# Kernel tuning notes

Measured on AMD Instinct MI355X. Metric: run time of the kernel, lower is better.

Reference implementation:

```python
import jax, jax.numpy as jnp
from jax import lax
import numpy as np

N_BLOCKS = 5; C = 256; K = 1024; NQ = 8; NRES = 4; B = 2; T = 65536


def conv1d(x, w, b, stride=1, padding=0, dilation=1):
    # x: [N,C,T], w: [O,I,k]
    y = lax.conv_general_dilated(x, w, (stride,), [(padding, padding)],
                                 rhs_dilation=(dilation,),
                                 dimension_numbers=('NCH', 'OIH', 'NCH'))
    return y + b[None, :, None]


def conv_transpose1d(x, w, b):
    # PyTorch ConvTranspose1d(k=4, s=2, p=1); w: [in, out, 4]
    wk = jnp.swapaxes(jnp.flip(w, -1), 0, 1)  # [out, in, 4]
    y = lax.conv_general_dilated(x, wk, (1,), [(2, 2)], lhs_dilation=(2,),
                                 dimension_numbers=('NCH', 'OIH', 'NCH'))
    return y + b[None, :, None]


def residual_model(x, w0, b0, w1, b1, dil):
    # ReLU -> dilated conv3 -> ReLU -> conv3
    h = conv1d(jax.nn.relu(x), w0, b0, padding=dil, dilation=dil)
    h = conv1d(jax.nn.relu(h), w1, b1, padding=1)
    return h


def encoder(x, d0w, d0b, dw, db, rw, rb):
    for i in range(N_BLOCKS):
        if i == 0:
            x = conv1d(x, d0w, d0b, stride=2, padding=1)
        else:
            x = conv1d(x, dw[i - 1], db[i - 1], stride=2, padding=1)
        for j in range(NRES):
            dil = 3 ** (j + 1)
            # ResidualBlock.forward: x + model(x)
            x = x + residual_model(x, rw[i, j, 0], rb[i, j, 0], rw[i, j, 1], rb[i, j, 1], dil)
    return x


def decoder(x, rw, rb, uw, ub, ulw, ulb):
    for i in range(N_BLOCKS):
        for j in range(NRES):
            dil = 3 ** (j + 1)
            # DecoderBlock: x = x + ResidualBlock(x) = x + (x + model(x))
            x = x + (x + residual_model(x, rw[i, j, 0], rb[i, j, 0], rw[i, j, 1], rb[i, j, 1], dil))
        if i == N_BLOCKS - 1:
            x = conv_transpose1d(x, ulw, ulb)
        else:
            x = conv_transpose1d(x, uw[i], ub[i])
    return x


def rvq(emb, rvq_sum, rvq_usage):
    # emb: [N, C]; eval-mode residual VQ (no EMA update)
    q = jnp.zeros_like(emb)
    commit = jnp.asarray(0.0, emb.dtype)
    codes = []
    for i in range(NQ):
        cb = rvq_sum[i] / jnp.clip(rvq_usage[i], 1e-5, None)[:, None]  # [K, C]
        res = emb - q
        # argmin of squared distance over codebook rows (||res||^2 constant per column)
        scores = jnp.sum(cb * cb, axis=1)[:, None] - 2.0 * (cb @ res.T)  # [K, N]
        c = jnp.argmin(scores, axis=0)
        eq = cb[c]  # [N, C]
        eq_st = res + lax.stop_gradient(eq - res)  # straight-through
        commit = commit + jnp.mean((lax.stop_gradient(eq_st) - res) ** 2)
        q = q + eq_st
        codes.append(c.astype(jnp.int32))
    return jnp.stack(codes, axis=1), q, commit


def setup_inputs() -> dict:
    key = jax.random.key(0)
    ks = iter(jax.random.split(key, 16))

    def W(shape, fan_in):
        return (jax.random.normal(next(ks), shape, jnp.float32) / np.float32(np.sqrt(fan_in)))

    return {
        'x': jax.random.normal(next(ks), (B, 1, T), jnp.float32),
        'enc_down0_w': W((C, 1, 4), 4),
        'enc_down0_b': jnp.zeros((C,), jnp.float32),
        'enc_down_w': W((N_BLOCKS - 1, C, C, 4), C * 4),
        'enc_down_b': jnp.zeros((N_BLOCKS - 1, C), jnp.float32),
        'enc_res_w': W((N_BLOCKS, NRES, 2, C, C, 3), C * 3),
        'enc_res_b': jnp.zeros((N_BLOCKS, NRES, 2, C), jnp.float32),
        'dec_res_w': W((N_BLOCKS, NRES, 2, C, C, 3), C * 3),
        'dec_res_b': jnp.zeros((N_BLOCKS, NRES, 2, C), jnp.float32),
        'dec_up_w': W((N_BLOCKS - 1, C, C, 4), C * 4),
        'dec_up_b': jnp.zeros((N_BLOCKS - 1, C), jnp.float32),
        'dec_up_last_w': W((C, 1, 4), C * 4),
        'dec_up_last_b': jnp.zeros((1,), jnp.float32),
        'rvq_sum': jax.random.normal(next(ks), (NQ, K, C), jnp.float32) * 0.1,
        'rvq_usage': jnp.ones((NQ, K), jnp.float32),
    }


def reference(x, enc_down0_w, enc_down0_b, enc_down_w, enc_down_b, enc_res_w, enc_res_b,
              dec_res_w, dec_res_b, dec_up_w, dec_up_b, dec_up_last_w, dec_up_last_b,
              rvq_sum, rvq_usage):
    z = encoder(x, enc_down0_w, enc_down0_b, enc_down_w, enc_down_b, enc_res_w, enc_res_b)
    Bz, Cz, Tz = z.shape
    emb = jnp.transpose(z, (0, 2, 1)).reshape(Bz * Tz, Cz)  # (b t) c
    codes, q, commit = rvq(emb, rvq_sum, rvq_usage)
    zq = jnp.transpose(q.reshape(Bz, Tz, Cz), (0, 2, 1))  # b c t
    recon = decoder(zq, dec_res_w, dec_res_b, dec_up_w, dec_up_b, dec_up_last_w, dec_up_last_b)
    return recon, codes, commit
```

## Files before the change

kernel.cpp:

```cpp
#include <hip/hip_runtime.h>
#include <cstdint>

#define DEVFN static __device__ __forceinline__
typedef unsigned short ushort_t;
typedef unsigned int uint_t;
typedef short short8 __attribute__((ext_vector_type(8)));
typedef float f32x4 __attribute__((ext_vector_type(4)));

DEVFN float bf2f(ushort_t h) { return __uint_as_float(((uint_t)h) << 16); }
DEVFN ushort_t bfhi(float f) {
    uint_t u = __float_as_uint(f);
    u += 0x7fffu + ((u >> 16) & 1u);
    return (ushort_t)(u >> 16);
}
DEVFN void fsplit(float f, ushort_t& h, ushort_t& l) {
    h = bfhi(f);
    l = bfhi(f - bf2f(h));
}
DEVFN void relu_pair(uint_t& h, uint_t& l) {
    float f0 = bf2f((ushort_t)(h & 0xffffu)) + bf2f((ushort_t)(l & 0xffffu));
    float f1 = bf2f((ushort_t)(h >> 16)) + bf2f((ushort_t)(l >> 16));
    if (f0 <= 0.f) { h &= 0xffff0000u; l &= 0xffff0000u; }
    if (f1 <= 0.f) { h &= 0x0000ffffu; l &= 0x0000ffffu; }
}

__global__ __launch_bounds__(256)
void wprep3_k(const float* __restrict__ erw, const float* __restrict__ drw,
              ushort_t* __restrict__ wH, ushort_t* __restrict__ wL)
{
    const int gid = blockIdx.x * 256 + threadIdx.x;
    const int conv = gid >> 16;
    const int rem  = gid & 65535;
    const int co = rem >> 8, ci = rem & 255;
    const float* src = (conv < 40) ? (erw + (size_t)conv * 196608)
                                   : (drw + (size_t)(conv - 40) * 196608);
    const float* p = src + ((size_t)co * 256 + ci) * 3;
    ushort_t* oh = wH + (size_t)conv * 196608 + rem;
    ushort_t* ol = wL + (size_t)conv * 196608 + rem;
#pragma unroll
    for (int k = 0; k < 3; ++k) {
        ushort_t h, l; fsplit(p[k], h, l);
        oh[k * 65536] = h; ol[k * 65536] = l;
    }
}

__global__ __launch_bounds__(256)
void wprep4_k(const float* __restrict__ edw, const float* __restrict__ duw,
              ushort_t* __restrict__ wH, ushort_t* __restrict__ wL)
{
    const int gid = blockIdx.x * 256 + threadIdx.x;
    const int conv = gid >> 16;
    const int rem  = gid & 65535;
    const int co = rem >> 8, ci = rem & 255;
    ushort_t* oh = wH + (size_t)conv * 262144 + rem;
    ushort_t* ol = wL + (size_t)conv * 262144 + rem;
#pragma unroll
    for (int k = 0; k < 4; ++k) {
        float f;
        if (conv < 4)  f = edw[(size_t)conv * 262144 + ((size_t)co * 256 + ci) * 4 + k];
        else           f = duw[(size_t)(conv - 4) * 262144 + ((size_t)ci * 256 + co) * 4 + k];
        ushort_t h, l; fsplit(f, h, l);
        oh[k * 65536] = h; ol[k * 65536] = l;
    }
}

template<int TAPS, int STRIDE, bool RELU, int NT, int DMAX>
__global__ __launch_bounds__(256, (NT >= 8) ? 2 : 3)
void convs_k(const ushort_t* __restrict__ inH, const ushort_t* __restrict__ inL,
             const ushort_t* __restrict__ wH, const ushort_t* __restrict__ wL,
             const float* __restrict__ bias,
             const ushort_t* __restrict__ srcH, const ushort_t* __restrict__ srcL,
             float alpha,
             ushort_t* __restrict__ outH, ushort_t* __restrict__ outL,
             int Lin, int Lout, int dil, int pad)
{
    constexpr int ROWS = NT * 16;
    constexpr int SMAX = STRIDE * (ROWS - 1) + (TAPS - 1) * DMAX + 1;
    constexpr int XSB  = SMAX * 40 * 2;
    constexpr int ARENA = (2 * XSB > 16640) ? 2 * XSB : 16640;
    __shared__ __align__(16) char sarena[ARENA];
    ushort_t (*xsH)[40] = (ushort_t(*)[40])(sarena);
    ushort_t (*xsL)[40] = (ushort_t(*)[40])(sarena + XSB);

    const int tid = threadIdx.x;
    const int b = blockIdx.z;
    const int t0 = blockIdx.x * ROWS;
    const int wave = tid >> 6, lane = tid & 63;
    const int quad = lane >> 4, lr = lane & 15;
    const int cow = wave * 64;
    const size_t inbase = (size_t)b * Lin * 256;
    const int S = STRIDE * (ROWS - 1) + (TAPS - 1) * dil + 1;
    const int g0 = STRIDE * t0 - pad;

    f32x4 acc[4][NT];
#pragma unroll
    for (int m = 0; m < 4; ++m)
#pragma unroll
        for (int n = 0; n < NT; ++n) acc[m][n] = (f32x4)0.f;

    for (int chunk = 0; chunk < 8; ++chunk) {
        const int ci0 = chunk * 32;
        __syncthreads();
        for (int idx = tid; idx < S * 4; idx += 256) {
            const int s = idx >> 2, p = idx & 3;
            const int t = g0 + s;
            uint4 hv = make_uint4(0, 0, 0, 0), lv = hv;
            if (t >= 0 && t < Lin) {
                const size_t g = inbase + (size_t)t * 256 + ci0 + p * 8;
                hv = *(const uint4*)(inH + g);
                lv = *(const uint4*)(inL + g);
                if (RELU) {
                    relu_pair(hv.x, lv.x); relu_pair(hv.y, lv.y);
                    relu_pair(hv.z, lv.z); relu_pair(hv.w, lv.w);
                }
            }
            *(uint4*)&xsH[s][p * 8] = hv;
            *(uint4*)&xsL[s][p * 8] = lv;
        }
        __syncthreads();
#pragma unroll
        for (int tap = 0; tap < TAPS; ++tap) {
            const ushort_t* wHt = wH + (size_t)tap * 65536 + ci0 + quad * 8;
            const ushort_t* wLt = wL + (size_t)tap * 65536 + ci0 + quad * 8;
            short8 aH[4], aL[4];
#pragma unroll
            for (int m = 0; m < 4; ++m) {
                const int co = cow + m * 16 + lr;
                aH[m] = *(const short8*)(wHt + co * 256);
                aL[m] = *(const short8*)(wLt + co * 256);
            }
            const int rb = tap * dil;
#pragma unroll
            for (int n = 0; n < NT; ++n) {
                const int srow = STRIDE * (n * 16 + lr) + rb;
                const short8 bH = *(const short8*)&xsH[srow][quad * 8];
                const short8 bL = *(const short8*)&xsL[srow][quad * 8];
#pragma unroll
                for (int m = 0; m < 4; ++m)
                    acc[m][n] = __builtin_amdgcn_mfma_f32_16x16x32_bf16(aH[m], bH, acc[m][n], 0, 0, 0);
#pragma unroll
                for (int m = 0; m < 4; ++m)
                    acc[m][n] = __builtin_amdgcn_mfma_f32_16x16x32_bf16(aH[m], bL, acc[m][n], 0, 0, 0);
#pragma unroll
                for (int m = 0; m < 4; ++m)
                    acc[m][n] = __builtin_amdgcn_mfma_f32_16x16x32_bf16(aL[m], bH, acc[m][n], 0, 0, 0);
            }
        }
    }
    float4 bvv[4];
#pragma unroll
    for (int m = 0; m < 4; ++m)
        bvv[m] = *(const float4*)&bias[cow + m * 16 + quad * 4];
    __syncthreads();
    float (*ebuf)[260] = (float(*)[260])sarena;
#pragma unroll
    for (int n = 0; n < NT; ++n) {
#pragma unroll
        for (int m = 0; m < 4; ++m) {
            float4 v;
            v.x = acc[m][n][0] + bvv[m].x;
            v.y = acc[m][n][1] + bvv[m].y;
            v.z = acc[m][n][2] + bvv[m].z;
            v.w = acc[m][n][3] + bvv[m].w;
            *(float4*)&ebuf[lr][cow + m * 16 + quad * 4] = v;
        }
        __syncthreads();
        {
            const int row = tid >> 4;
            const int c00 = (tid & 15) * 4;
            const int t = t0 + n * 16 + row;
            const size_t gr = ((size_t)b * Lout + t) * 256;
#pragma unroll
            for (int rep = 0; rep < 4; ++rep) {
                const int col = c00 + rep * 64;
                float4 v = *(const float4*)&ebuf[row][col];
                if (alpha != 0.f) {
                    const ushort4 sh = *(const ushort4*)(srcH + gr + col);
                    const ushort4 sl = *(const ushort4*)(srcL + gr + col);
                    v.x += alpha * (bf2f(sh.x) + bf2f(sl.x));
                    v.y += alpha * (bf2f(sh.y) + bf2f(sl.y));
                    v.z += alpha * (bf2f(sh.z) + bf2f(sl.z));
                    v.w += alpha * (bf2f(sh.w) + bf2f(sl.w));
                }
                ushort4 oh, ol;
                fsplit(v.x, oh.x, ol.x); fsplit(v.y, oh.y, ol.y);
                fsplit(v.z, oh.z, ol.z); fsplit(v.w, oh.w, ol.w);
                *(ushort4*)(outH + gr + col) = oh;
                *(ushort4*)(outL + gr + col) = ol;
            }
        }
        __syncthreads();
    }
}

template<int NTc>
__global__ __launch_bounds__(256, 2)
void convt_k(const ushort_t* __restrict__ inH, const ushort_t* __restrict__ inL,
             const ushort_t* __restrict__ wH, const ushort_t* __restrict__ wL,
             const float* __restrict__ bias,
             ushort_t* __restrict__ outH, ushort_t* __restrict__ outL, int Lin)
{
    constexpr int ROWS = NTc * 16;
    constexpr int S = ROWS + 2;
    constexpr int XSB = S * 40 * 2;
    constexpr int ARENA = (2 * XSB > 33280) ? 2 * XSB : 33280;
    __shared__ __align__(16) char sarena[ARENA];
    ushort_t (*xsH)[40] = (ushort_t(*)[40])(sarena);
    ushort_t (*xsL)[40] = (ushort_t(*)[40])(sarena + XSB);

    const int tid = threadIdx.x;
    const int b = blockIdx.z;
    const int m0 = blockIdx.x * ROWS;
    const int Lout = Lin * 2;
    const int wave = tid >> 6, lane = tid & 63;
    const int quad = lane >> 4, lr = lane & 15;
    const int cow = wave * 64;
    const size_t inbase = (size_t)b * Lin * 256;

    f32x4 acc[4][NTc][2];
#pragma unroll
    for (int m = 0; m < 4; ++m)
#pragma unroll
        for (int n = 0; n < NTc; ++n) { acc[m][n][0] = (f32x4)0.f; acc[m][n][1] = (f32x4)0.f; }

    for (int chunk = 0; chunk < 8; ++chunk) {
        const int ci0 = chunk * 32;
        __syncthreads();
        for (int idx = tid; idx < S * 4; idx += 256) {
            const int s = idx >> 2, p = idx & 3;
            const int t = m0 - 1 + s;
            uint4 hv = make_uint4(0, 0, 0, 0), lv = hv;
            if (t >= 0 && t < Lin) {
                const size_t g = inbase + (size_t)t * 256 + ci0 + p * 8;
                hv = *(const uint4*)(inH + g);
                lv = *(const uint4*)(inL + g);
            }
            *(uint4*)&xsH[s][p * 8] = hv;
            *(uint4*)&xsL[s][p * 8] = lv;
        }
        __syncthreads();
#pragma unroll
        for (int tap = 0; tap < 4; ++tap) {
            const int ph = (tap == 0 || tap == 2) ? 1 : 0;
            const int sh = (tap == 0) ? 1 : ((tap == 3) ? -1 : 0);
            const ushort_t* wHt = wH + (size_t)tap * 65536 + ci0 + quad * 8;
            const ushort_t* wLt = wL + (size_t)tap * 65536 + ci0 + quad * 8;
            short8 aH[4], aL[4];
#pragma unroll
            for (int m = 0; m < 4; ++m) {
                const int co = cow + m * 16 + lr;
                aH[m] = *(const short8*)(wHt + co * 256);
                aL[m] = *(const short8*)(wLt + co * 256);
            }
#pragma unroll
            for (int n = 0; n < NTc; ++n) {
                const int srow = n * 16 + lr + sh + 1;
                const short8 bH = *(const short8*)&xsH[srow][quad * 8];
                const short8 bL = *(const short8*)&xsL[srow][quad * 8];
#pragma unroll
                for (int m = 0; m < 4; ++m)
                    acc[m][n][ph] = __builtin_amdgcn_mfma_f32_16x16x32_bf16(aH[m], bH, acc[m][n][ph], 0, 0, 0);
#pragma unroll
                for (int m = 0; m < 4; ++m)
                    acc[m][n][ph] = __builtin_amdgcn_mfma_f32_16x16x32_bf16(aH[m], bL, acc[m][n][ph], 0, 0, 0);
#pragma unroll
                for (int m = 0; m < 4; ++m)
                    acc[m][n][ph] = __builtin_amdgcn_mfma_f32_16x16x32_bf16(aL[m], bH, acc[m][n][ph], 0, 0, 0);
            }
        }
    }
    float4 bvv[4];
#pragma unroll
    for (int m = 0; m < 4; ++m)
        bvv[m] = *(const float4*)&bias[cow + m * 16 + quad * 4];
    __syncthreads();
    float (*ebuf)[260] = (float(*)[260])sarena;
#pragma unroll
    for (int n = 0; n < NTc; ++n) {
#pragma unroll
        for (int m = 0; m < 4; ++m) {
#pragma unroll
            for (int ph = 0; ph < 2; ++ph) {
                float4 v;
                v.x = acc[m][n][ph][0] + bvv[m].x;
                v.y = acc[m][n][ph][1] + bvv[m].y;
                v.z = acc[m][n][ph][2] + bvv[m].z;
                v.w = acc[m][n][ph][3] + bvv[m].w;
                *(float4*)&ebuf[2 * lr + ph][cow + m * 16 + quad * 4] = v;
            }
        }
        __syncthreads();
        {
            const int baset = 2 * (m0 + n * 16);
#pragma unroll
            for (int h = 0; h < 8; ++h) {
                const int row = (tid >> 4) + 16 * (h >> 2);
                const int col = (tid & 15) * 4 + (h & 3) * 64;
                const int t = baset + row;
                const size_t gr = ((size_t)b * Lout + t) * 256 + col;
                float4 v = *(const float4*)&ebuf[row][col];
                ushort4 oh, ol;
                fsplit(v.x, oh.x, ol.x); fsplit(v.y, oh.y, ol.y);
                fsplit(v.z, oh.z, ol.z); fsplit(v.w, oh.w, ol.w);
                *(ushort4*)(outH + gr) = oh;
                *(ushort4*)(outL + gr) = ol;
            }
        }
        __syncthreads();
    }
}

__global__ __launch_bounds__(256)
void down0_k2(const float* __restrict__ x, const float* __restrict__ w,
              const float* __restrict__ bias,
              ushort_t* __restrict__ outH, ushort_t* __restrict__ outL)
{
    const int t = blockIdx.x;
    const int b = blockIdx.y;
    const int co = threadIdx.x;
    const float* xb = x + (size_t)b * 65536;
    const float4 wv = *(const float4*)(w + co * 4);
    float s = bias[co];
    const int ti0 = 2 * t - 1;
    if (ti0 >= 0)      s = fmaf(xb[ti0], wv.x, s);
    s = fmaf(xb[ti0 + 1], wv.y, s);
    s = fmaf(xb[ti0 + 2], wv.z, s);
    if (ti0 + 3 < 65536) s = fmaf(xb[ti0 + 3], wv.w, s);
    ushort_t h, l; fsplit(s, h, l);
    const size_t g = ((size_t)b * 32768 + t) * 256 + co;
    outH[g] = h; outL[g] = l;
}

__global__ __launch_bounds__(256)
void uplast_k2(const ushort_t* __restrict__ inH, const ushort_t* __restrict__ inL,
               const float* __restrict__ w, const float* __restrict__ bias,
               float* __restrict__ out, int Lin)
{
    const int m = blockIdx.x * 256 + threadIdx.x;
    const int b = blockIdx.y;
    const float bv = bias[0];
    float aE = bv, aO = bv;
    const size_t base = (size_t)b * Lin * 256;
    const ushort_t* r0H = inH + base + (size_t)m * 256;
    const ushort_t* r0L = inL + base + (size_t)m * 256;
    const bool hasM = (m > 0), hasP = (m + 1 < Lin);
    for (int c0 = 0; c0 < 256; c0 += 8) {
        uint4 h0 = *(const uint4*)(r0H + c0);
        uint4 l0 = *(const uint4*)(r0L + c0);
        uint4 hm = make_uint4(0,0,0,0), lm = hm, hp = hm, lp = hm;
        if (hasM) { hm = *(const uint4*)(r0H - 256 + c0); lm = *(const uint4*)(r0L - 256 + c0); }
        if (hasP) { hp = *(const uint4*)(r0H + 256 + c0); lp = *(const uint4*)(r0L + 256 + c0); }
        const uint_t* h0p = (const uint_t*)&h0; const uint_t* l0p = (const uint_t*)&l0;
        const uint_t* hmp = (const uint_t*)&hm; const uint_t* lmp = (const uint_t*)&lm;
        const uint_t* hpp = (const uint_t*)&hp; const uint_t* lpp = (const uint_t*)&lp;
#pragma unroll
        for (int e = 0; e < 4; ++e) {
#pragma unroll
            for (int half = 0; half < 2; ++half) {
                const int sh = half * 16;
                const int ci = c0 + e * 2 + half;
                const float x0  = bf2f((ushort_t)(h0p[e] >> sh)) + bf2f((ushort_t)(l0p[e] >> sh));
                const float xm1 = bf2f((ushort_t)(hmp[e] >> sh)) + bf2f((ushort_t)(lmp[e] >> sh));
                const float xp1 = bf2f((ushort_t)(hpp[e] >> sh)) + bf2f((ushort_t)(lpp[e] >> sh));
                const float4 wv = *(const float4*)(w + ci * 4);
                aE = fmaf(x0, wv.y, fmaf(xm1, wv.w, aE));
                aO = fmaf(xp1, wv.x, fmaf(x0, wv.z, aO));
            }
        }
    }
    *(float2*)(out + (size_t)b * 2 * Lin + 2 * m) = make_float2(aE, aO);
}

__global__ void emb_k(const ushort_t* __restrict__ H, const ushort_t* __restrict__ L,
                      float* __restrict__ emb)
{
    const size_t g = (size_t)blockIdx.x * 256 + threadIdx.x;
    emb[g] = bf2f(H[g]) + bf2f(L[g]);
}
__global__ void qsplit_k(const float* __restrict__ q,
                         ushort_t* __restrict__ H, ushort_t* __restrict__ L)
{
    const size_t g = (size_t)blockIdx.x * 256 + threadIdx.x;
    ushort_t h, l; fsplit(q[g], h, l);
    H[g] = h; L[g] = l;
}

__global__ __launch_bounds__(256)
void rvq_cb_k(const float* __restrict__ sum, const float* __restrict__ usage,
              float* __restrict__ cb, float* __restrict__ cbT,
              float* __restrict__ cbn, int iq)
{
    const int k = blockIdx.x, c = threadIdx.x;
    const float den = fmaxf(usage[iq * 1024 + k], 1e-5f);
    const float v = sum[((size_t)iq * 1024 + k) * 256 + c] / den;
    cb[(size_t)k * 256 + c] = v;
    cbT[(size_t)c * 1024 + k] = v;
    float s = v * v;
    for (int off = 32; off; off >>= 1) s += __shfl_down(s, off, 64);
    __shared__ float ls[4];
    if ((c & 63) == 0) ls[c >> 6] = s;
    __syncthreads();
    if (c == 0) cbn[k] = ls[0] + ls[1] + ls[2] + ls[3];
}

DEVFN unsigned int ordbits(float f)
{
    unsigned u = __float_as_uint(f);
    return (u & 0x80000000u) ? ~u : (u | 0x80000000u);
}
DEVFN unsigned long long shfl_xor_u64(unsigned long long v, int mask)
{
    int lo = (int)(v & 0xffffffffull), hi = (int)(v >> 32);
    lo = __shfl_xor(lo, mask, 64);
    hi = __shfl_xor(hi, mask, 64);
    return ((unsigned long long)(unsigned)hi << 32) | (unsigned)lo;
}

__global__ __launch_bounds__(256)
void rvq_argmin_k(const float* __restrict__ emb, const float* __restrict__ q,
                  const float* __restrict__ cbT, const float* __restrict__ cbn,
                  int* __restrict__ codes, float* __restrict__ codes_out, int iq)
{
    const int n0 = blockIdx.x * 16;
    const int tid = threadIdx.x;
    __shared__ float res[16][256];
    for (int idx = tid; idx < 16 * 256; idx += 256) {
        int nl = idx >> 8, c = idx & 255;
        size_t g = (size_t)(n0 + nl) * 256 + c;
        res[nl][c] = emb[g] - q[g];
    }
    __syncthreads();
    float dot[16][4];
#pragma unroll
    for (int nl = 0; nl < 16; ++nl)
#pragma unroll
        for (int j = 0; j < 4; ++j) dot[nl][j] = 0.f;

    const float* cbtp = cbT + tid * 4;
    for (int c = 0; c < 256; ++c) {
        const float4 cbv = *(const float4*)(cbtp + (size_t)c * 1024);
#pragma unroll
        for (int nl = 0; nl < 16; ++nl) {
            const float r = res[nl][c];
            dot[nl][0] = fmaf(cbv.x, r, dot[nl][0]);
            dot[nl][1] = fmaf(cbv.y, r, dot[nl][1]);
            dot[nl][2] = fmaf(cbv.z, r, dot[nl][2]);
            dot[nl][3] = fmaf(cbv.w, r, dot[nl][3]);
        }
    }
    const float4 nrm = *(const float4*)(cbn + tid * 4);
    __shared__ unsigned long long wred[4][16];
    const int wave = tid >> 6, lane = tid & 63;
#pragma unroll
    for (int nl = 0; nl < 16; ++nl) {
        float s0 = nrm.x - 2.f * dot[nl][0];
        float s1 = nrm.y - 2.f * dot[nl][1];
        float s2 = nrm.z - 2.f * dot[nl][2];
        float s3 = nrm.w - 2.f * dot[nl][3];
        unsigned long long key =
            ((unsigned long long)ordbits(s0) << 32) | (unsigned)(tid * 4 + 0);
        unsigned long long k1 =
            ((unsigned long long)ordbits(s1) << 32) | (unsigned)(tid * 4 + 1);
        unsigned long long k2 =
            ((unsigned long long)ordbits(s2) << 32) | (unsigned)(tid * 4 + 2);
        unsigned long long k3 =
            ((unsigned long long)ordbits(s3) << 32) | (unsigned)(tid * 4 + 3);
        if (k1 < key) key = k1;
        if (k2 < key) key = k2;
        if (k3 < key) key = k3;
        for (int off = 32; off; off >>= 1) {
            unsigned long long o = shfl_xor_u64(key, off);
            if (o < key) key = o;
        }
        if (lane == 0) wred[wave][nl] = key;
    }
    __syncthreads();
    if (tid < 16) {
        unsigned long long bkey = wred[0][tid];
        if (wred[1][tid] < bkey) bkey = wred[1][tid];
        if (wred[2][tid] < bkey) bkey = wred[2][tid];
        if (wred[3][tid] < bkey) bkey = wred[3][tid];
        const int code = (int)(bkey & 0xffffffffull);
        codes[(size_t)(n0 + tid) * 8 + iq] = code;
        codes_out[(size_t)(n0 + tid) * 8 + iq] = (float)code;
    }
}

__global__ __launch_bounds__(256)
void rvq_update_k(const float* __restrict__ emb, float* __restrict__ q,
                  const float* __restrict__ cb, const int* __restrict__ codes,
                  float* __restrict__ commit, int iq)
{
    const int n = blockIdx.x, c = threadIdx.x;
    const int code = codes[(size_t)n * 8 + iq];
    const size_t g = (size_t)n * 256 + c;
    const float qv = q[g] + cb[(size_t)code * 256 + c];
    q[g] = qv;
    const float e = qv - emb[g];
    float s = e * e;
    for (int off = 32; off; off >>= 1) s += __shfl_down(s, off, 64);
    __shared__ float ls[4];
    if ((c & 63) == 0) ls[c >> 6] = s;
    __syncthreads();
    if (c == 0) atomicAdd(commit, ls[0] + ls[1] + ls[2] + ls[3]);
}

__global__ void commit_write_k(const float* __restrict__ commit, float* __restrict__ out)
{
    out[0] = commit[0] * (1.f / (4096.f * 256.f));
}

extern "C" void kernel_launch(void* const* d_in, const int* in_sizes, int n_in,
                              void* d_out, int out_size, void* d_ws, size_t ws_size,
                              hipStream_t stream)
{
    const float* x    = (const float*)d_in[0];
    const float* ed0w = (const float*)d_in[1];
    const float* ed0b = (const float*)d_in[2];
    const float* edw  = (const float*)d_in[3];
    const float* edb  = (const float*)d_in[4];
    const float* erw  = (const float*)d_in[5];
    const float* erb  = (const float*)d_in[6];
    const float* drw  = (const float*)d_in[7];
    const float* drb  = (const float*)d_in[8];
    const float* duw  = (const float*)d_in[9];
    const float* dub  = (const float*)d_in[10];
    const float* dulw = (const float*)d_in[11];
    const float* dulb = (const float*)d_in[12];
    const float* rsum = (const float*)d_in[13];
    const float* rusg = (const float*)d_in[14];
    float* out = (float*)d_out;

    char* base = (char*)d_ws;
    size_t o = 0;
    ushort_t* wH3 = (ushort_t*)(base + o); o += 31457280;
    ushort_t* wL3 = (ushort_t*)(base + o); o += 31457280;
    ushort_t* w4H = (ushort_t*)(base + o); o += 4194304;
    ushort_t* w4L = (ushort_t*)(base + o); o += 4194304;
    ushort_t* AH  = (ushort_t*)(base + o); o += 33554432;
    ushort_t* AL  = (ushort_t*)(base + o); o += 33554432;
    ushort_t* BH  = (ushort_t*)(base + o); o += 33554432;
    ushort_t* BL  = (ushort_t*)(base + o); o += 33554432;
    float* emb    = (float*)(base + o);    o += 4194304;
    float* q      = (float*)(base + o);    o += 4194304;
    float* commit = (float*)(base + o);    o += 64;
    float* cb     = (float*)(base + o);    o += 1048576;
    float* cbT    = (float*)(base + o);    o += 1048576;
    float* cbn    = (float*)(base + o);    o += 4096;
    int*   codes  = (int*)(base + o);      o += 131072;

    static const int DIL[4] = {3, 9, 27, 81};

    hipMemsetAsync(q, 0, 4194304 + 64, stream);

    wprep3_k<<<20480, 256, 0, stream>>>(erw, drw, wH3, wL3);
    wprep4_k<<<2048, 256, 0, stream>>>(edw, duw, w4H, w4L);

    auto conv3 = [&](const ushort_t* iH, const ushort_t* iL,
                     const ushort_t* wh, const ushort_t* wl, const float* bb,
                     const ushort_t* sH, const ushort_t* sL, float alpha,
                     ushort_t* oH, ushort_t* oL, int L, int d) {
        if (L >= 16384)
            convs_k<3, 1, true, 8, 81><<<dim3(L / 128, 1, 2), 256, 0, stream>>>(
                iH, iL, wh, wl, bb, sH, sL, alpha, oH, oL, L, L, d, d);
        else if (L >= 8192)
            convs_k<3, 1, true, 4, 81><<<dim3(L / 64, 1, 2), 256, 0, stream>>>(
                iH, iL, wh, wl, bb, sH, sL, alpha, oH, oL, L, L, d, d);
        else if (L >= 4096)
            convs_k<3, 1, true, 2, 81><<<dim3(L / 32, 1, 2), 256, 0, stream>>>(
                iH, iL, wh, wl, bb, sH, sL, alpha, oH, oL, L, L, d, d);
        else
            convs_k<3, 1, true, 1, 81><<<dim3(L / 16, 1, 2), 256, 0, stream>>>(
                iH, iL, wh, wl, bb, sH, sL, alpha, oH, oL, L, L, d, d);
    };

    down0_k2<<<dim3(32768, 2), 256, 0, stream>>>(x, ed0w, ed0b, AH, AL);
    int L = 32768;
    for (int i = 0; i < 5; ++i) {
        if (i > 0) {
            const ushort_t* wh = w4H + (size_t)(i - 1) * 262144;
            const ushort_t* wl = w4L + (size_t)(i - 1) * 262144;
            const int Lout = L / 2;
            if (Lout >= 16384)
                convs_k<4, 2, false, 8, 1><<<dim3(Lout / 128, 1, 2), 256, 0, stream>>>(
                    AH, AL, wh, wl, edb + (i - 1) * 256, AH, AL, 0.f, BH, BL, L, Lout, 1, 1);
            else if (Lout >= 8192)
                convs_k<4, 2, false, 4, 1><<<dim3(Lout / 64, 1, 2), 256, 0, stream>>>(
                    AH, AL, wh, wl, edb + (i - 1) * 256, AH, AL, 0.f, BH, BL, L, Lout, 1, 1);
            else if (Lout >= 4096)
                convs_k<4, 2, false, 2, 1><<<dim3(Lout / 32, 1, 2), 256, 0, stream>>>(
                    AH, AL, wh, wl, edb + (i - 1) * 256, AH, AL, 0.f, BH, BL, L, Lout, 1, 1);
            else
                convs_k<4, 2, false, 1, 1><<<dim3(Lout / 16, 1, 2), 256, 0, stream>>>(
                    AH, AL, wh, wl, edb + (i - 1) * 256, AH, AL, 0.f, BH, BL, L, Lout, 1, 1);
            ushort_t* t;
            t = AH; AH = BH; BH = t;
            t = AL; AL = BL; BL = t;
            L = Lout;
        }
        for (int j = 0; j < 4; ++j) {
            const int d = DIL[j];
            const size_t u = (size_t)(i * 4 + j) * 2;
            conv3(AH, AL, wH3 + (u + 0) * 196608, wL3 + (u + 0) * 196608,
                  erb + (u + 0) * 256, AH, AL, 0.f, BH, BL, L, d);
            conv3(BH, BL, wH3 + (u + 1) * 196608, wL3 + (u + 1) * 196608,
                  erb + (u + 1) * 256, AH, AL, 1.f, AH, AL, L, 1);
        }
    }

    emb_k<<<4096, 256, 0, stream>>>(AH, AL, emb);
    for (int iq = 0; iq < 8; ++iq) {
        rvq_cb_k<<<1024, 256, 0, stream>>>(rsum, rusg, cb, cbT, cbn, iq);
        rvq_argmin_k<<<256, 256, 0, stream>>>(emb, q, cbT, cbn, codes, out + 131072, iq);
        rvq_update_k<<<4096, 256, 0, stream>>>(emb, q, cb, codes, commit, iq);
    }
    qsplit_k<<<4096, 256, 0, stream>>>(q, AH, AL);

    L = 2048;
    for (int i = 0; i < 5; ++i) {
        for (int j = 0; j < 4; ++j) {
            const int d = DIL[j];
            const size_t u = 40 + (size_t)(i * 4 + j) * 2;
            conv3(AH, AL, wH3 + (u + 0) * 196608, wL3 + (u + 0) * 196608,
                  drb + ((size_t)(i * 4 + j) * 2 + 0) * 256, AH, AL, 0.f, BH, BL, L, d);
            conv3(BH, BL, wH3 + (u + 1) * 196608, wL3 + (u + 1) * 196608,
                  drb + ((size_t)(i * 4 + j) * 2 + 1) * 256, AH, AL, 2.f, AH, AL, L, 1);
        }
        if (i < 4) {
            const ushort_t* wh = w4H + (size_t)(4 + i) * 262144;
            const ushort_t* wl = w4L + (size_t)(4 + i) * 262144;
            if (L >= 16384)
                convt_k<4><<<dim3(L / 64, 1, 2), 256, 0, stream>>>(
                    AH, AL, wh, wl, dub + i * 256, BH, BL, L);
            else if (L >= 8192)
                convt_k<4><<<dim3(L / 64, 1, 2), 256, 0, stream>>>(
                    AH, AL, wh, wl, dub + i * 256, BH, BL, L);
            else if (L >= 4096)
                convt_k<2><<<dim3(L / 32, 1, 2), 256, 0, stream>>>(
                    AH, AL, wh, wl, dub + i * 256, BH, BL, L);
            else
                convt_k<1><<<dim3(L / 16, 1, 2), 256, 0, stream>>>(
                    AH, AL, wh, wl, dub + i * 256, BH, BL, L);
            ushort_t* t;
            t = AH; AH = BH; BH = t;
            t = AL; AL = BL; BL = t;
            L *= 2;
        } else {
            uplast_k2<<<dim3(L / 256, 2), 256, 0, stream>>>(AH, AL, dulw, dulb, out, L);
        }
    }

    commit_write_k<<<1, 1, 0, stream>>>(commit, out + 163840);
}
```

Measured before the change: 6.055 ms.

## Double-buffer input tiles in dilated conv kernel to overlap loads with MFMA

New measurement: 6.007 ms. Within noise of the previous version (-0.8%).

```diff
diff --git a/kernel.cpp b/kernel.cpp
--- a/kernel.cpp
+++ b/kernel.cpp
@@ -64,7 +64,7 @@
     }
 }
 
-template<int TAPS, int STRIDE, bool RELU, int NT, int DMAX>
+template<int TAPS, int STRIDE, bool RELU, int NT, int DMAX, bool DBUF>
 __global__ __launch_bounds__(256, (NT >= 8) ? 2 : 3)
 void convs_k(const ushort_t* __restrict__ inH, const ushort_t* __restrict__ inL,
              const ushort_t* __restrict__ wH, const ushort_t* __restrict__ wL,
@@ -76,11 +76,11 @@
 {
     constexpr int ROWS = NT * 16;
     constexpr int SMAX = STRIDE * (ROWS - 1) + (TAPS - 1) * DMAX + 1;
-    constexpr int XSB  = SMAX * 40 * 2;
-    constexpr int ARENA = (2 * XSB > 16640) ? 2 * XSB : 16640;
+    constexpr int XSB  = SMAX * 80;
+    constexpr int NEED = DBUF ? 4 * XSB : 2 * XSB;
+    constexpr int ARENA = (NEED > 16640) ? NEED : 16640;
+    static_assert(!DBUF || (4 * SMAX <= TAPS * 256), "prefetch item budget");
     __shared__ __align__(16) char sarena[ARENA];
-    ushort_t (*xsH)[40] = (ushort_t(*)[40])(sarena);
-    ushort_t (*xsL)[40] = (ushort_t(*)[40])(sarena + XSB);
 
     const int tid = threadIdx.x;
     const int b = blockIdx.z;
@@ -98,15 +98,17 @@
 #pragma unroll
         for (int n = 0; n < NT; ++n) acc[m][n] = (f32x4)0.f;
 
-    for (int chunk = 0; chunk < 8; ++chunk) {
-        const int ci0 = chunk * 32;
-        __syncthreads();
+    if constexpr (DBUF) {
+        ushort_t (*xsH0)[40] = (ushort_t(*)[40])(sarena);
+        ushort_t (*xsL0)[40] = (ushort_t(*)[40])(sarena + XSB);
+        ushort_t (*xsH1)[40] = (ushort_t(*)[40])(sarena + 2 * XSB);
+        ushort_t (*xsL1)[40] = (ushort_t(*)[40])(sarena + 3 * XSB);
         for (int idx = tid; idx < S * 4; idx += 256) {
             const int s = idx >> 2, p = idx & 3;
             const int t = g0 + s;
             uint4 hv = make_uint4(0, 0, 0, 0), lv = hv;
             if (t >= 0 && t < Lin) {
-                const size_t g = inbase + (size_t)t * 256 + ci0 + p * 8;
+                const size_t g = inbase + (size_t)t * 256 + p * 8;
                 hv = *(const uint4*)(inH + g);
                 lv = *(const uint4*)(inL + g);
                 if (RELU) {
@@ -114,36 +116,115 @@
                     relu_pair(hv.z, lv.z); relu_pair(hv.w, lv.w);
                 }
             }
-            *(uint4*)&xsH[s][p * 8] = hv;
-            *(uint4*)&xsL[s][p * 8] = lv;
+            *(uint4*)&xsH0[s][p * 8] = hv;
+            *(uint4*)&xsL0[s][p * 8] = lv;
         }
         __syncthreads();
-#pragma unroll
-        for (int tap = 0; tap < TAPS; ++tap) {
-            const ushort_t* wHt = wH + (size_t)tap * 65536 + ci0 + quad * 8;
-            const ushort_t* wLt = wL + (size_t)tap * 65536 + ci0 + quad * 8;
-            short8 aH[4], aL[4];
-#pragma unroll
-            for (int m = 0; m < 4; ++m) {
-                const int co = cow + m * 16 + lr;
-                aH[m] = *(const short8*)(wHt + co * 256);
-                aL[m] = *(const short8*)(wLt + co * 256);
-            }
-            const int rb = tap * dil;
-#pragma unroll
-            for (int n = 0; n < NT; ++n) {
-                const int srow = STRIDE * (n * 16 + lr) + rb;
-                const short8 bH = *(const short8*)&xsH[srow][quad * 8];
-                const short8 bL = *(const short8*)&xsL[srow][quad * 8];
-#pragma unroll
-                for (int m = 0; m < 4; ++m)
-                    acc[m][n] = __builtin_amdgcn_mfma_f32_16x16x32_bf16(aH[m], bH, acc[m][n], 0, 0, 0);
-#pragma unroll
-                for (int m = 0; m < 4; ++m)
-                    acc[m][n] = __builtin_amdgcn_mfma_f32_16x16x32_bf16(aH[m], bL, acc[m][n], 0, 0, 0);
-#pragma unroll
-                for (int m = 0; m < 4; ++m)
-                    acc[m][n] = __builtin_amdgcn_mfma_f32_16x16x32_bf16(aL[m], bH, acc[m][n], 0, 0, 0);
+        for (int chunk = 0; chunk < 8; ++chunk) {
+            const int ci0 = chunk * 32;
+            ushort_t (*xsH)[40] = (chunk & 1) ? xsH1 : xsH0;
+            ushort_t (*xsL)[40] = (chunk & 1) ? xsL1 : xsL0;
+            ushort_t (*xnH)[40] = (chunk & 1) ? xsH0 : xsH1;
+            ushort_t (*xnL)[40] = (chunk & 1) ? xsL0 : xsL1;
+            const bool pf = (chunk < 7);
+#pragma unroll
+            for (int tap = 0; tap < TAPS; ++tap) {
+                const ushort_t* wHt = wH + (size_t)tap * 65536 + ci0 + quad * 8;
+                const ushort_t* wLt = wL + (size_t)tap * 65536 + ci0 + quad * 8;
+                short8 aH[4], aL[4];
+#pragma unroll
+                for (int m = 0; m < 4; ++m) {
+                    const int co = cow + m * 16 + lr;
+                    aH[m] = *(const short8*)(wHt + co * 256);
+                    aL[m] = *(const short8*)(wLt + co * 256);
+                }
+                const int idx = tap * 256 + tid;
+                const int s = idx >> 2, p = idx & 3;
+                const int tr = g0 + s;
+                const bool inr = (idx < S * 4);
+                uint4 hv = make_uint4(0, 0, 0, 0), lv = hv;
+                if (pf && inr && tr >= 0 && tr < Lin) {
+                    const size_t g = inbase + (size_t)tr * 256 + (ci0 + 32) + p * 8;
+                    hv = *(const uint4*)(inH + g);
+                    lv = *(const uint4*)(inL + g);
+                }
+                const int rb = tap * dil;
+#pragma unroll
+                for (int n = 0; n < NT; ++n) {
+                    const int srow = STRIDE * (n * 16 + lr) + rb;
+                    const short8 bH = *(const short8*)&xsH[srow][quad * 8];
+                    const short8 bL = *(const short8*)&xsL[srow][quad * 8];
+#pragma unroll
+                    for (int m = 0; m < 4; ++m)
+                        acc[m][n] = __builtin_amdgcn_mfma_f32_16x16x32_bf16(aH[m], bH, acc[m][n], 0, 0, 0);
+#pragma unroll
+                    for (int m = 0; m < 4; ++m)
+                        acc[m][n] = __builtin_amdgcn_mfma_f32_16x16x32_bf16(aH[m], bL, acc[m][n], 0, 0, 0);
+#pragma unroll
+                    for (int m = 0; m < 4; ++m)
+                        acc[m][n] = __builtin_amdgcn_mfma_f32_16x16x32_bf16(aL[m], bH, acc[m][n], 0, 0, 0);
+                }
+                if (pf && inr) {
+                    if (RELU) {
+                        relu_pair(hv.x, lv.x); relu_pair(hv.y, lv.y);
+                        relu_pair(hv.z, lv.z); relu_pair(hv.w, lv.w);
+                    }
+                    *(uint4*)&xnH[s][p * 8] = hv;
+                    *(uint4*)&xnL[s][p * 8] = lv;
+                }
+            }
+            __syncthreads();
+        }
+    } else {
+        ushort_t (*xsH)[40] = (ushort_t(*)[40])(sarena);
+        ushort_t (*xsL)[40] = (ushort_t(*)[40])(sarena + XSB);
+        for (int chunk = 0; chunk < 8; ++chunk) {
+            const int ci0 = chunk * 32;
+            __syncthreads();
+            for (int idx = tid; idx < S * 4; idx += 256) {
+                const int s = idx >> 2, p = idx & 3;
+                const int t = g0 + s;
+                uint4 hv = make_uint4(0, 0, 0, 0), lv = hv;
+                if (t >= 0 && t < Lin) {
+                    const size_t g = inbase + (size_t)t * 256 + ci0 + p * 8;
+                    hv = *(const uint4*)(inH + g);
+                    lv = *(const uint4*)(inL + g);
+                    if (RELU) {
+                        relu_pair(hv.x, lv.x); relu_pair(hv.y, lv.y);
+                        relu_pair(hv.z, lv.z); relu_pair(hv.w, lv.w);
+                    }
+                }
+                *(uint4*)&xsH[s][p * 8] = hv;
+                *(uint4*)&xsL[s][p * 8] = lv;
+            }
+            __syncthreads();
+#pragma unroll
+            for (int tap = 0; tap < TAPS; ++tap) {
+                const ushort_t* wHt = wH + (size_t)tap * 65536 + ci0 + quad * 8;
+                const ushort_t* wLt = wL + (size_t)tap * 65536 + ci0 + quad * 8;
+                short8 aH[4], aL[4];
+#pragma unroll
+                for (int m = 0; m < 4; ++m) {
+                    const int co = cow + m * 16 + lr;
+                    aH[m] = *(const short8*)(wHt + co * 256);
+                    aL[m] = *(const short8*)(wLt + co * 256);
+                }
+                const int rb = tap * dil;
+#pragma unroll
+                for (int n = 0; n < NT; ++n) {
+                    const int srow = STRIDE * (n * 16 + lr) + rb;
+                    const short8 bH = *(const short8*)&xsH[srow][quad * 8];
+                    const short8 bL = *(const short8*)&xsL[srow][quad * 8];
+#pragma unroll
+                    for (int m = 0; m < 4; ++m)
+                        acc[m][n] = __builtin_amdgcn_mfma_f32_16x16x32_bf16(aH[m], bH, acc[m][n], 0, 0, 0);
+#pragma unroll
+                    for (int m = 0; m < 4; ++m)
+                        acc[m][n] = __builtin_amdgcn_mfma_f32_16x16x32_bf16(aH[m], bL, acc[m][n], 0, 0, 0);
+#pragma unroll
+                    for (int m = 0; m < 4; ++m)
+                        acc[m][n] = __builtin_amdgcn_mfma_f32_16x16x32_bf16(aL[m], bH, acc[m][n], 0, 0, 0);
+                }
             }
         }
     }
@@ -560,18 +641,28 @@
                      const ushort_t* wh, const ushort_t* wl, const float* bb,
                      const ushort_t* sH, const ushort_t* sL, float alpha,
                      ushort_t* oH, ushort_t* oL, int L, int d) {
-        if (L >= 16384)
-            convs_k<3, 1, true, 8, 81><<<dim3(L / 128, 1, 2), 256, 0, stream>>>(
-                iH, iL, wh, wl, bb, sH, sL, alpha, oH, oL, L, L, d, d);
-        else if (L >= 8192)
-            convs_k<3, 1, true, 4, 81><<<dim3(L / 64, 1, 2), 256, 0, stream>>>(
-                iH, iL, wh, wl, bb, sH, sL, alpha, oH, oL, L, L, d, d);
-        else if (L >= 4096)
-            convs_k<3, 1, true, 2, 81><<<dim3(L / 32, 1, 2), 256, 0, stream>>>(
-                iH, iL, wh, wl, bb, sH, sL, alpha, oH, oL, L, L, d, d);
-        else
-            convs_k<3, 1, true, 1, 81><<<dim3(L / 16, 1, 2), 256, 0, stream>>>(
-                iH, iL, wh, wl, bb, sH, sL, alpha, oH, oL, L, L, d, d);
+        const bool db = (d <= 27);
+        if (L >= 16384) {
+            if (db) convs_k<3, 1, true, 8, 27, true><<<dim3(L / 128, 1, 2), 256, 0, stream>>>(
+                        iH, iL, wh, wl, bb, sH, sL, alpha, oH, oL, L, L, d, d);
+            else    convs_k<3, 1, true, 8, 81, false><<<dim3(L / 128, 1, 2), 256, 0, stream>>>(
+                        iH, iL, wh, wl, bb, sH, sL, alpha, oH, oL, L, L, d, d);
+        } else if (L >= 8192) {
+            if (db) convs_k<3, 1, true, 4, 27, true><<<dim3(L / 64, 1, 2), 256, 0, stream>>>(
+                        iH, iL, wh, wl, bb, sH, sL, alpha, oH, oL, L, L, d, d);
+            else    convs_k<3, 1, true, 4, 81, false><<<dim3(L / 64, 1, 2), 256, 0, stream>>>(
+                        iH, iL, wh, wl, bb, sH, sL, alpha, oH, oL, L, L, d, d);
+        } else if (L >= 4096) {
+            if (db) convs_k<3, 1, true, 2, 27, true><<<dim3(L / 32, 1, 2), 256, 0, stream>>>(
+                        iH, iL, wh, wl, bb, sH, sL, alpha, oH, oL, L, L, d, d);
+            else    convs_k<3, 1, true, 2, 81, false><<<dim3(L / 32, 1, 2), 256, 0, stream>>>(
+                        iH, iL, wh, wl, bb, sH, sL, alpha, oH, oL, L, L, d, d);
+        } else {
+            if (db) convs_k<3, 1, true, 1, 27, true><<<dim3(L / 16, 1, 2), 256, 0, stream>>>(
+                        iH, iL, wh, wl, bb, sH, sL, alpha, oH, oL, L, L, d, d);
+            else    convs_k<3, 1, true, 1, 81, false><<<dim3(L / 16, 1, 2), 256, 0, stream>>>(
+                        iH, iL, wh, wl, bb, sH, sL, alpha, oH, oL, L, L, d, d);
+        }
     };
 
     down0_k2<<<dim3(32768, 2), 256, 0, stream>>>(x, ed0w, ed0b, AH, AL);
@@ -582,16 +673,16 @@
             const ushort_t* wl = w4L + (size_t)(i - 1) * 262144;
             const int Lout = L / 2;
             if (Lout >= 16384)
-                convs_k<4, 2, false, 8, 1><<<dim3(Lout / 128, 1, 2), 256, 0, stream>>>(
+                convs_k<4, 2, false, 8, 1, false><<<dim3(Lout / 128, 1, 2), 256, 0, stream>>>(
                     AH, AL, wh, wl, edb + (i - 1) * 256, AH, AL, 0.f, BH, BL, L, Lout, 1, 1);
             else if (Lout >= 8192)
-                convs_k<4, 2, false, 4, 1><<<dim3(Lout / 64, 1, 2), 256, 0, stream>>>(
+                convs_k<4, 2, false, 4, 1, false><<<dim3(Lout / 64, 1, 2), 256, 0, stream>>>(
                     AH, AL, wh, wl, edb + (i - 1) * 256, AH, AL, 0.f, BH, BL, L, Lout, 1, 1);
             else if (Lout >= 4096)
-                convs_k<4, 2, false, 2, 1><<<dim3(Lout / 32, 1, 2), 256, 0, stream>>>(
+                convs_k<4, 2, false, 2, 1, false><<<dim3(Lout / 32, 1, 2), 256, 0, stream>>>(
                     AH, AL, wh, wl, edb + (i - 1) * 256, AH, AL, 0.f, BH, BL, L, Lout, 1, 1);
             else
-                convs_k<4, 2, false, 1, 1><<<dim3(Lout / 16, 1, 2), 256, 0, stream>>>(
+                convs_k<4, 2, false, 1, 1, false><<<dim3(Lout / 16, 1, 2), 256, 0, stream>>>(
                     AH, AL, wh, wl, edb + (i - 1) * 256, AH, AL, 0.f, BH, BL, L, Lout, 1, 1);
             ushort_t* t;
             t = AH; AH = BH; BH = t;
@@ -629,10 +720,7 @@
         if (i < 4) {
             const ushort_t* wh = w4H + (size_t)(4 + i) * 262144;
             const ushort_t* wl = w4L + (size_t)(4 + i) * 262144;
-            if (L >= 16384)
-                convt_k<4><<<dim3(L / 64, 1, 2), 256, 0, stream>>>(
-                    AH, AL, wh, wl, dub + i * 256, BH, BL, L);
-            else if (L >= 8192)
+            if (L >= 8192)
                 convt_k<4><<<dim3(L / 64, 1, 2), 256, 0, stream>>>(
                     AH, AL, wh, wl, dub + i * 256, BH, BL, L);
             else if (L >= 4096)
```
